# Performance work log

Measured on AMD Instinct MI355X. Metric: run time of the kernel, lower is better.

## Reference

```python
import jax, jax.numpy as jnp
import numpy as np

N_NODES = 100000


def setup_inputs() -> dict:
    key = jax.random.key(0)
    k1, k2, k3, k4, k5 = jax.random.split(key, 5)
    h = jax.random.normal(k1, (N_NODES, 128), dtype=jnp.float32)
    norm = jax.random.uniform(k2, (N_NODES, 1), dtype=jnp.float32)  # D^{-1/2}-style per-node norm
    W = jax.random.normal(k3, (128, 64), dtype=jnp.float32) * 0.05
    b = jnp.zeros((64,), dtype=jnp.float32)
    src = jax.random.randint(k4, (1600000,), 0, N_NODES, dtype=jnp.int32)
    dst = jax.random.randint(k5, (1600000,), 0, N_NODES, dtype=jnp.int32)
    return {"h": h, "norm": norm, "W": W, "b": b, "src": src, "dst": dst}


def reference(h, norm, W, b, src, dst):
    # Dense feature transform: g.ndata['h'] = h @ W   (dropout is identity at inference)
    hw = jnp.matmul(h, W)  # [N, out]
    # Message: src feature scaled by src norm
    msg = hw[src] * norm[src]  # [E, out]
    # Reduce: sum messages into dst, scale by dst norm
    agg = jax.ops.segment_sum(msg, dst, num_segments=N_NODES) * norm  # [N, out]
    out = agg + b
    return jax.nn.relu(out)
```

## Files before the change

kernel.cpp:

```cpp
#include <hip/hip_runtime.h>


typedef unsigned int u32;
typedef unsigned short u16;
typedef __attribute__((ext_vector_type(8))) short s16x8;
typedef __attribute__((ext_vector_type(4))) float f32x4;

#define NB_LOG 7
#define NPB 128
#define CAP 4096
#define MAXB 1024
#define EPB 8192
#define RT 512

__device__ __forceinline__ float bf2f(u16 v) {
  return __uint_as_float(((u32)v) << 16);
}
__device__ __forceinline__ u16 f2bf(float f) {
  u32 u = __float_as_uint(f);
  return (u16)((u + 0x7fffu + ((u >> 16) & 1u)) >> 16);
}

__global__ __launch_bounds__(256) void wconv(
    const float* __restrict__ W, u16* __restrict__ Wtg, u32* __restrict__ gcur) {
  int o = blockIdx.x * 256 + threadIdx.x;
  int j = o & 7, col = (o >> 3) & 15, kq = (o >> 7) & 3, ks = (o >> 9) & 3,
      ct = (o >> 11) & 3;
  int k = ks * 32 + kq * 8 + j;
  int n = ct * 16 + col;
  Wtg[o] = f2bf(W[k * 64 + n]);
  if (o < MAXB) gcur[o] = 0;
}

__global__ __launch_bounds__(256) void gemm_mfma(
    const float* __restrict__ h, const float* __restrict__ norm,
    const u16* __restrict__ Wtg, u16* __restrict__ scaledh, int N) {
  int lane = threadIdx.x & 63, wid = threadIdx.x >> 6;
  int col = lane & 15, kq = lane >> 4;

  s16x8 bfrag[4][4];
#pragma unroll
  for (int ct = 0; ct < 4; ++ct)
#pragma unroll
    for (int ks = 0; ks < 4; ++ks) {
      int f = ct * 16 + ks * 4 + kq;
      bfrag[ct][ks] = *reinterpret_cast<const s16x8*>(Wtg + ((size_t)(f * 16 + col) * 8));
    }

  int row0 = blockIdx.x * 64 + wid * 16;
  int myrow = row0 + col;
  int ldrow = myrow < N ? myrow : (N - 1);
  const float* __restrict__ hrow = h + (size_t)ldrow * 128 + kq * 8;

  f32x4 acc[4];
#pragma unroll
  for (int ct = 0; ct < 4; ++ct) acc[ct] = (f32x4){0.f, 0.f, 0.f, 0.f};

#pragma unroll
  for (int ks = 0; ks < 4; ++ks) {
    float4 x0 = *reinterpret_cast<const float4*>(hrow + ks * 32);
    float4 x1 = *reinterpret_cast<const float4*>(hrow + ks * 32 + 4);
    s16x8 a;
    a[0] = (short)f2bf(x0.x); a[1] = (short)f2bf(x0.y);
    a[2] = (short)f2bf(x0.z); a[3] = (short)f2bf(x0.w);
    a[4] = (short)f2bf(x1.x); a[5] = (short)f2bf(x1.y);
    a[6] = (short)f2bf(x1.z); a[7] = (short)f2bf(x1.w);
#pragma unroll
    for (int ct = 0; ct < 4; ++ct)
      acc[ct] = __builtin_amdgcn_mfma_f32_16x16x32_bf16(a, bfrag[ct][ks], acc[ct], 0, 0, 0);
  }

#pragma unroll
  for (int reg = 0; reg < 4; ++reg) {
    int node = row0 + kq * 4 + reg;
    if (node < N) {
      float nm = norm[node];
#pragma unroll
      for (int ct = 0; ct < 4; ++ct)
        scaledh[(size_t)node * 64 + ct * 16 + col] = f2bf(acc[ct][reg] * nm);
    }
  }
}

__global__ __launch_bounds__(1024) void bin_edges(
    const int* __restrict__ src, const int* __restrict__ dst,
    u32* __restrict__ gcur, u32* __restrict__ bins, int E) {
  __shared__ u32 lhist[MAXB];
  __shared__ u32 lbase[MAXB];
  int t = threadIdx.x;
  for (int i = t; i < MAXB; i += 1024) lhist[i] = 0;
  __syncthreads();
  int e0 = blockIdx.x * EPB;
  int s[8], d[8];
  u32 r[8];
#pragma unroll
  for (int k = 0; k < 8; ++k) {
    int e = e0 + k * 1024 + t;
    bool ok = e < E;
    s[k] = ok ? src[e] : 0;
    d[k] = ok ? dst[e] : -1;
  }
#pragma unroll
  for (int k = 0; k < 8; ++k) {
    if (d[k] >= 0) r[k] = atomicAdd(&lhist[d[k] >> NB_LOG], 1u);
  }
  __syncthreads();
  for (int i = t; i < MAXB; i += 1024) {
    u32 c = lhist[i];
    lbase[i] = c ? atomicAdd(&gcur[i], c) : 0u;
  }
  __syncthreads();
#pragma unroll
  for (int k = 0; k < 8; ++k) {
    if (d[k] >= 0) {
      int bk = d[k] >> NB_LOG;
      u32 p = lbase[bk] + r[k];
      if (p < CAP)
        bins[(size_t)bk * CAP + p] = ((u32)s[k] << NB_LOG) | (u32)(d[k] & (NPB - 1));
    }
  }
}

__global__ __launch_bounds__(RT) void bucket_reduce(
    const u16* __restrict__ scaledh, const u32* __restrict__ bins,
    const u32* __restrict__ gcur, const float* __restrict__ norm,
    const float* __restrict__ bias, float* __restrict__ out, int N) {
  __shared__ u32 hist[NPB];
  __shared__ u32 tmp[NPB];
  __shared__ u32 startp[NPB + 1];
  __shared__ u32 sorted[CAP];
  int bkt = blockIdx.x;
  int t = threadIdx.x, lane = t & 63, wid = t >> 6;
  int cnt = (int)gcur[bkt];
  if (cnt > CAP) cnt = CAP;
  for (int i = t; i < NPB; i += RT) hist[i] = 0;
  __syncthreads();

  const u32* __restrict__ my = bins + (size_t)bkt * CAP;
  u32 w[CAP / RT];
  u32 rk[CAP / RT];
#pragma unroll
  for (int k = 0; k < CAP / RT; ++k) {
    int e = k * RT + t;
    w[k] = (e < cnt) ? my[e] : 0xFFFFFFFFu;
  }
#pragma unroll
  for (int k = 0; k < CAP / RT; ++k) {
    if (w[k] != 0xFFFFFFFFu)
      rk[k] = atomicAdd(&hist[w[k] & (NPB - 1)], 1u);
  }
  __syncthreads();
  if (t < NPB) tmp[t] = hist[t];
  __syncthreads();
  for (int off = 1; off < NPB; off <<= 1) {
    u32 x = (t < NPB && t >= off) ? tmp[t - off] : 0;
    __syncthreads();
    if (t < NPB) tmp[t] += x;
    __syncthreads();
  }
  if (t < NPB) startp[t] = tmp[t] - hist[t];
  if (t == NPB - 1) startp[NPB] = tmp[NPB - 1];
  __syncthreads();
#pragma unroll
  for (int k = 0; k < CAP / RT; ++k) {
    if (w[k] != 0xFFFFFFFFu)
      sorted[startp[w[k] & (NPB - 1)] + rk[k]] = w[k] >> NB_LOG;
  }
  __syncthreads();

  float bl = bias[lane];
  int base = bkt << NB_LOG;
  for (int r = wid; r < NPB; r += RT / 64) {
    int node = base + r;
    if (node >= N) break;
    int beg = (int)startp[r], end = (int)startp[r + 1];
    float a0 = 0.f, a1 = 0.f, a2 = 0.f, a3 = 0.f;
    int j = beg;
    for (; j + 4 <= end; j += 4) {
      int s0 = (int)sorted[j];
      int s1 = (int)sorted[j + 1];
      int s2 = (int)sorted[j + 2];
      int s3 = (int)sorted[j + 3];
      a0 += bf2f(scaledh[(size_t)s0 * 64 + lane]);
      a1 += bf2f(scaledh[(size_t)s1 * 64 + lane]);
      a2 += bf2f(scaledh[(size_t)s2 * 64 + lane]);
      a3 += bf2f(scaledh[(size_t)s3 * 64 + lane]);
    }
    for (; j < end; ++j)
      a0 += bf2f(scaledh[(size_t)sorted[j] * 64 + lane]);
    float acc = (a0 + a1) + (a2 + a3);
    out[(size_t)node * 64 + lane] = fmaxf(fmaf(acc, norm[node], bl), 0.f);
  }
}

__global__ __launch_bounds__(256) void zero_out(float4* __restrict__ o4, size_t n4) {
  size_t tid = blockIdx.x * 256 + threadIdx.x;
  size_t stride = (size_t)gridDim.x * 256;
  for (size_t i = tid; i < n4; i += stride) o4[i] = make_float4(0.f, 0.f, 0.f, 0.f);
}

__global__ __launch_bounds__(256) void scatter_edges(
    const u16* __restrict__ scaledh, const int* __restrict__ src,
    const int* __restrict__ dst, float* __restrict__ agg, int E) {
  int lane = threadIdx.x & 63;
  int gwid = (blockIdx.x * 256 + threadIdx.x) >> 6;
  int nw = (gridDim.x * 256) >> 6;
  for (int e = gwid; e < E; e += nw) {
    int s = __builtin_amdgcn_readfirstlane(src[e]);
    int d = __builtin_amdgcn_readfirstlane(dst[e]);
    float v = bf2f(scaledh[(size_t)s * 64 + lane]);
    unsafeAtomicAdd(&agg[(size_t)d * 64 + lane], v);
  }
}

__global__ __launch_bounds__(256) void finalize(
    float4* __restrict__ out4, const float* __restrict__ norm,
    const float4* __restrict__ b4, int N) {
  size_t total4 = (size_t)N * 16;
  size_t tid = blockIdx.x * 256 + threadIdx.x;
  size_t stride = (size_t)gridDim.x * 256;
  for (size_t t = tid; t < total4; t += stride) {
    int i = (int)(t >> 4), q = (int)(t & 15);
    float4 v = out4[t];
    float nm = norm[i];
    float4 bb = b4[q];
    v.x = fmaxf(fmaf(v.x, nm, bb.x), 0.f);
    v.y = fmaxf(fmaf(v.y, nm, bb.y), 0.f);
    v.z = fmaxf(fmaf(v.z, nm, bb.z), 0.f);
    v.w = fmaxf(fmaf(v.w, nm, bb.w), 0.f);
    out4[t] = v;
  }
}

extern "C" void kernel_launch(void* const* d_in, const int* in_sizes, int n_in,
                              void* d_out, int out_size, void* d_ws, size_t ws_size,
                              hipStream_t stream) {
  const float* h    = (const float*)d_in[0];
  const float* norm = (const float*)d_in[1];
  const float* W    = (const float*)d_in[2];
  const float* b    = (const float*)d_in[3];
  const int*   src  = (const int*)d_in[4];
  const int*   dst  = (const int*)d_in[5];

  int N = in_sizes[1];
  int E = in_sizes[4];
  int nbuckets = (N + NPB - 1) >> NB_LOG;
  int nrb = (N + 63) >> 6;

  char* ws = (char*)d_ws;
  size_t off = 0;
  u16* scaledh = (u16*)(ws + off); off += (((size_t)N * 64 * 2) + 255) & ~(size_t)255;
  u32* gcur    = (u32*)(ws + off); off += (MAXB * 4 + 255) & ~(size_t)255;
  u16* Wtg     = (u16*)(ws + off); off += (8192 * 2 + 255) & ~(size_t)255;
  u32* bins    = (u32*)(ws + off); off += (size_t)MAXB * CAP * 4;
  size_t needed = off;
  size_t needed_fb = (size_t)((char*)bins - ws);

  if (ws_size >= needed && nbuckets <= MAXB) {
    wconv<<<32, 256, 0, stream>>>(W, Wtg, gcur);
    gemm_mfma<<<nrb, 256, 0, stream>>>(h, norm, Wtg, scaledh, N);
    bin_edges<<<(E + EPB - 1) / EPB, 1024, 0, stream>>>(src, dst, gcur, bins, E);
    bucket_reduce<<<nbuckets, RT, 0, stream>>>(scaledh, bins, gcur, norm, b,
                                               (float*)d_out, N);
  } else if (ws_size >= needed_fb) {
    float* agg = (float*)d_out;
    wconv<<<32, 256, 0, stream>>>(W, Wtg, gcur);
    gemm_mfma<<<nrb, 256, 0, stream>>>(h, norm, Wtg, scaledh, N);
    zero_out<<<1024, 256, 0, stream>>>((float4*)agg, (size_t)N * 16);
    scatter_edges<<<2048, 256, 0, stream>>>(scaledh, src, dst, agg, E);
    finalize<<<1024, 256, 0, stream>>>((float4*)agg, norm, (const float4*)b, N);
  }
}
```

Before: 90.38 us.

## Shrink buckets and gather four edges per wave with vectorized bf16 loads

Bucket size drops from 128 nodes to 64 nodes, with a 256-thread block per bucket, so more blocks are launched and each uses less shared memory. The multi-barrier LDS prefix scan becomes a single-wave shuffle scan. The gather loop now splits each wave into four 16-lane groups. Each lane loads four bf16 values at once, so four edges are processed per step, and two destination rows are interleaved to raise memory-level parallelism. Partial sums are combined with xor shuffles, and output is written as float4, at the cost of more shuffle work and divergent loop tails.

```diff
diff --git a/kernel.cpp b/kernel.cpp
--- a/kernel.cpp
+++ b/kernel.cpp
@@ -6,12 +6,12 @@
 typedef __attribute__((ext_vector_type(8))) short s16x8;
 typedef __attribute__((ext_vector_type(4))) float f32x4;
 
-#define NB_LOG 7
-#define NPB 128
-#define CAP 4096
-#define MAXB 1024
+#define NB_LOG 6
+#define NPB 64
+#define CAP 2048
+#define MAXB 2048
 #define EPB 8192
-#define RT 512
+#define RT 256
 
 __device__ __forceinline__ float bf2f(u16 v) {
   return __uint_as_float(((u32)v) << 16);
@@ -124,16 +124,15 @@
 __global__ __launch_bounds__(RT) void bucket_reduce(
     const u16* __restrict__ scaledh, const u32* __restrict__ bins,
     const u32* __restrict__ gcur, const float* __restrict__ norm,
-    const float* __restrict__ bias, float* __restrict__ out, int N) {
+    const float4* __restrict__ bias4, float* __restrict__ out, int N) {
   __shared__ u32 hist[NPB];
-  __shared__ u32 tmp[NPB];
   __shared__ u32 startp[NPB + 1];
   __shared__ u32 sorted[CAP];
   int bkt = blockIdx.x;
   int t = threadIdx.x, lane = t & 63, wid = t >> 6;
   int cnt = (int)gcur[bkt];
   if (cnt > CAP) cnt = CAP;
-  for (int i = t; i < NPB; i += RT) hist[i] = 0;
+  if (t < NPB) hist[t] = 0;
   __syncthreads();
 
   const u32* __restrict__ my = bins + (size_t)bkt * CAP;
@@ -150,16 +149,17 @@
       rk[k] = atomicAdd(&hist[w[k] & (NPB - 1)], 1u);
   }
   __syncthreads();
-  if (t < NPB) tmp[t] = hist[t];
-  __syncthreads();
-  for (int off = 1; off < NPB; off <<= 1) {
-    u32 x = (t < NPB && t >= off) ? tmp[t - off] : 0;
-    __syncthreads();
-    if (t < NPB) tmp[t] += x;
-    __syncthreads();
-  }
-  if (t < NPB) startp[t] = tmp[t] - hist[t];
-  if (t == NPB - 1) startp[NPB] = tmp[NPB - 1];
+  if (t < NPB) {
+    u32 v = hist[t];
+    u32 inc = v;
+#pragma unroll
+    for (int m = 1; m < NPB; m <<= 1) {
+      u32 x = __shfl_up(inc, m);
+      if (t >= m) inc += x;
+    }
+    startp[t] = inc - v;
+    if (t == NPB - 1) startp[NPB] = inc;
+  }
   __syncthreads();
 #pragma unroll
   for (int k = 0; k < CAP / RT; ++k) {
@@ -168,28 +168,63 @@
   }
   __syncthreads();
 
-  float bl = bias[lane];
+  int grp = lane >> 4, c4 = lane & 15;
+  float4 bl = bias4[c4];
   int base = bkt << NB_LOG;
-  for (int r = wid; r < NPB; r += RT / 64) {
-    int node = base + r;
-    if (node >= N) break;
-    int beg = (int)startp[r], end = (int)startp[r + 1];
-    float a0 = 0.f, a1 = 0.f, a2 = 0.f, a3 = 0.f;
-    int j = beg;
-    for (; j + 4 <= end; j += 4) {
-      int s0 = (int)sorted[j];
-      int s1 = (int)sorted[j + 1];
-      int s2 = (int)sorted[j + 2];
-      int s3 = (int)sorted[j + 3];
-      a0 += bf2f(scaledh[(size_t)s0 * 64 + lane]);
-      a1 += bf2f(scaledh[(size_t)s1 * 64 + lane]);
-      a2 += bf2f(scaledh[(size_t)s2 * 64 + lane]);
-      a3 += bf2f(scaledh[(size_t)s3 * 64 + lane]);
-    }
-    for (; j < end; ++j)
-      a0 += bf2f(scaledh[(size_t)sorted[j] * 64 + lane]);
-    float acc = (a0 + a1) + (a2 + a3);
-    out[(size_t)node * 64 + lane] = fmaxf(fmaf(acc, norm[node], bl), 0.f);
+  for (int rr = wid; rr < NPB; rr += 8) {
+    int rA = rr, rB = rr + 4;
+    int nodeA = base + rA, nodeB = base + rB;
+    int jA = (int)startp[rA] + grp, endA = (int)startp[rA + 1];
+    int jB = (int)startp[rB] + grp, endB = (int)startp[rB + 1];
+    float4 aA = make_float4(0.f, 0.f, 0.f, 0.f);
+    float4 aB = make_float4(0.f, 0.f, 0.f, 0.f);
+    while (jA < endA || jB < endB) {
+      if (jA < endA) {
+        int s = (int)sorted[jA];
+        uint2 v = *reinterpret_cast<const uint2*>(scaledh + (size_t)s * 64 + c4 * 4);
+        aA.x += __uint_as_float(v.x << 16);
+        aA.y += __uint_as_float(v.x & 0xFFFF0000u);
+        aA.z += __uint_as_float(v.y << 16);
+        aA.w += __uint_as_float(v.y & 0xFFFF0000u);
+        jA += 4;
+      }
+      if (jB < endB) {
+        int s = (int)sorted[jB];
+        uint2 v = *reinterpret_cast<const uint2*>(scaledh + (size_t)s * 64 + c4 * 4);
+        aB.x += __uint_as_float(v.x << 16);
+        aB.y += __uint_as_float(v.x & 0xFFFF0000u);
+        aB.z += __uint_as_float(v.y << 16);
+        aB.w += __uint_as_float(v.y & 0xFFFF0000u);
+        jB += 4;
+      }
+    }
+#pragma unroll
+    for (int m = 16; m <= 32; m <<= 1) {
+      aA.x += __shfl_xor(aA.x, m); aA.y += __shfl_xor(aA.y, m);
+      aA.z += __shfl_xor(aA.z, m); aA.w += __shfl_xor(aA.w, m);
+      aB.x += __shfl_xor(aB.x, m); aB.y += __shfl_xor(aB.y, m);
+      aB.z += __shfl_xor(aB.z, m); aB.w += __shfl_xor(aB.w, m);
+    }
+    if (grp == 0) {
+      if (nodeA < N) {
+        float nm = norm[nodeA];
+        float4 o;
+        o.x = fmaxf(fmaf(aA.x, nm, bl.x), 0.f);
+        o.y = fmaxf(fmaf(aA.y, nm, bl.y), 0.f);
+        o.z = fmaxf(fmaf(aA.z, nm, bl.z), 0.f);
+        o.w = fmaxf(fmaf(aA.w, nm, bl.w), 0.f);
+        *reinterpret_cast<float4*>(out + (size_t)nodeA * 64 + c4 * 4) = o;
+      }
+      if (nodeB < N) {
+        float nm = norm[nodeB];
+        float4 o;
+        o.x = fmaxf(fmaf(aB.x, nm, bl.x), 0.f);
+        o.y = fmaxf(fmaf(aB.y, nm, bl.y), 0.f);
+        o.z = fmaxf(fmaf(aB.z, nm, bl.z), 0.f);
+        o.w = fmaxf(fmaf(aB.w, nm, bl.w), 0.f);
+        *reinterpret_cast<float4*>(out + (size_t)nodeB * 64 + c4 * 4) = o;
+      }
+    }
   }
 }
 
@@ -260,8 +295,8 @@
     wconv<<<32, 256, 0, stream>>>(W, Wtg, gcur);
     gemm_mfma<<<nrb, 256, 0, stream>>>(h, norm, Wtg, scaledh, N);
     bin_edges<<<(E + EPB - 1) / EPB, 1024, 0, stream>>>(src, dst, gcur, bins, E);
-    bucket_reduce<<<nbuckets, RT, 0, stream>>>(scaledh, bins, gcur, norm, b,
-                                               (float*)d_out, N);
+    bucket_reduce<<<nbuckets, RT, 0, stream>>>(scaledh, bins, gcur, norm,
+                                               (const float4*)b, (float*)d_out, N);
   } else if (ws_size >= needed_fb) {
     float* agg = (float*)d_out;
     wconv<<<32, 256, 0, stream>>>(W, Wtg, gcur);
```

Measured after the change: 88.28 us. -2.3%, faster.
